# Kernel tuning notes

Hardware: AMD Instinct MI355X
Metric: run time of the kernel (lower is better)

Reference implementation:

```python
import jax, jax.numpy as jnp
import numpy as np

N_NODES = 50000
N_EDGES = 800000
IN_CH, HID, LAT = 256, 128, 64


def setup_inputs() -> dict:
    key = jax.random.key(0)
    k1, k2, k3, k4 = jax.random.split(key, 4)
    x = jax.random.normal(k1, (N_NODES, IN_CH), dtype=jnp.float32)
    edge_index = jax.random.randint(k2, (2, N_EDGES), 0, N_NODES, dtype=jnp.int64)
    W1 = jax.random.normal(k3, (IN_CH, HID), dtype=jnp.float32) * (1.0 / np.sqrt(IN_CH))
    b1 = jnp.zeros((HID,), dtype=jnp.float32)
    W2 = jax.random.normal(k4, (HID, LAT), dtype=jnp.float32) * (1.0 / np.sqrt(HID))
    b2 = jnp.zeros((LAT,), dtype=jnp.float32)
    return {"x": x, "edge_index": edge_index, "W1": W1, "b1": b1, "W2": W2, "b2": b2}


def gcn_conv(x, src, dst, deg_inv_sqrt, W, b):
    # PyG GCNConv: h = x @ W; out[dst] += d_dst^-1/2 * d_src^-1/2 * h[src]; + bias
    h = x @ W                                   # [N, out]
    norm = deg_inv_sqrt[src] * deg_inv_sqrt[dst]  # [E+N]
    msg = h[src] * norm[:, None]                # [E+N, out] (gather + scale)
    out = jax.ops.segment_sum(msg, dst, num_segments=x.shape[0])
    return out + b


def reference(x, edge_index, W1, b1, W2, b2):
    n = x.shape[0]
    loop = jnp.arange(n, dtype=edge_index.dtype)
    # add self loops (GCNConv default)
    src = jnp.concatenate([edge_index[0], loop])
    dst = jnp.concatenate([edge_index[1], loop])
    deg = jax.ops.segment_sum(jnp.ones_like(dst, dtype=x.dtype), dst, num_segments=n)
    deg_inv_sqrt = jnp.where(deg > 0, jax.lax.rsqrt(deg), 0.0)
    h = jax.nn.relu(gcn_conv(x, src, dst, deg_inv_sqrt, W1, b1))
    h = jax.nn.relu(gcn_conv(h, src, dst, deg_inv_sqrt, W2, b2))
    return h
```

## Files before the change

### kernel.cpp

```cpp
#include <hip/hip_runtime.h>

#define N_NODES 50000
#define N_EDGES 800000
#define IN_CH 256
#define HID 128
#define LAT 64
#define CAP 64
#define NBIN 196
#define BINCAP 4864

typedef __attribute__((ext_vector_type(8))) short short8;
typedef __attribute__((ext_vector_type(16))) float f32x16;

static __device__ __forceinline__ unsigned short bf16_rne(float x) {
    unsigned u = __float_as_uint(x);
    unsigned r = (u + 0x7FFFu + ((u >> 16) & 1u)) >> 16;
    return (unsigned short)r;
}
static __device__ __forceinline__ float bf16_to_f(unsigned short h) {
    return __uint_as_float(((unsigned)h) << 16);
}

static __device__ __forceinline__ void add8(uint4 p, float* a) {
    a[0] += __uint_as_float(p.x << 16);
    a[1] += __uint_as_float(p.x & 0xFFFF0000u);
    a[2] += __uint_as_float(p.y << 16);
    a[3] += __uint_as_float(p.y & 0xFFFF0000u);
    a[4] += __uint_as_float(p.z << 16);
    a[5] += __uint_as_float(p.z & 0xFFFF0000u);
    a[6] += __uint_as_float(p.w << 16);
    a[7] += __uint_as_float(p.w & 0xFFFF0000u);
}
static __device__ __forceinline__ void fma8(uint4 p, float m, float* a) {
    a[0] = fmaf(m, __uint_as_float(p.x << 16), a[0]);
    a[1] = fmaf(m, __uint_as_float(p.x & 0xFFFF0000u), a[1]);
    a[2] = fmaf(m, __uint_as_float(p.y << 16), a[2]);
    a[3] = fmaf(m, __uint_as_float(p.y & 0xFFFF0000u), a[3]);
    a[4] = fmaf(m, __uint_as_float(p.z << 16), a[4]);
    a[5] = fmaf(m, __uint_as_float(p.z & 0xFFFF0000u), a[5]);
    a[6] = fmaf(m, __uint_as_float(p.w << 16), a[6]);
    a[7] = fmaf(m, __uint_as_float(p.w & 0xFFFF0000u), a[7]);
}

template <int K, int NN>
static __device__ __forceinline__ void split_store(const float* __restrict__ W,
                                                   unsigned short* __restrict__ Wf, int i) {
    constexpr int CT = NN / 32;
    int k = i / NN, n = i % NN;
    float w = W[i];
    unsigned short hi = bf16_rne(w);
    unsigned short lo = bf16_rne(w - bf16_to_f(hi));
    size_t off = ((size_t)((k >> 4) * CT + (n >> 5)) * 64 + ((n & 31) + 32 * ((k >> 3) & 1))) * 8 + (k & 7);
    Wf[off] = hi;
    Wf[(size_t)K * NN + off] = lo;
}

__global__ __launch_bounds__(256) void prep_kernel(const float* __restrict__ W1,
                                                   const float* __restrict__ W2,
                                                   int* __restrict__ binCnt,
                                                   unsigned short* __restrict__ W1f,
                                                   unsigned short* __restrict__ W2f) {
    int i = blockIdx.x * blockDim.x + threadIdx.x;
    if (i < NBIN) binCnt[i] = 0;
    if (i < IN_CH * HID) split_store<IN_CH, HID>(W1, W1f, i);
    if (i < HID * LAT) split_store<HID, LAT>(W2, W2f, i);
}

__global__ __launch_bounds__(256) void fill1_kernel(const int* __restrict__ ei,
                                                    int* __restrict__ binCnt,
                                                    unsigned int* __restrict__ binBuf, int E) {
    __shared__ int hist[NBIN];
    __shared__ int base[NBIN];
    const int tid = threadIdx.x;
    for (int i = tid; i < NBIN; i += 256) hist[i] = 0;
    __syncthreads();

    const int e0 = blockIdx.x * 2048 + tid;
    unsigned int pk[8];
    int bn[8], ofs[8];
#pragma unroll
    for (int i = 0; i < 8; ++i) {
        int e = e0 + 256 * i;
        bool v = e < E;
        int s = v ? ei[e] : 0;
        int d = v ? ei[E + e] : 0;
        bn[i] = d >> 8;
        pk[i] = (unsigned int)s | ((unsigned int)(d & 255) << 16);
        ofs[i] = v ? atomicAdd(&hist[bn[i]], 1) : -1;
    }
    __syncthreads();
    for (int i = tid; i < NBIN; i += 256)
        base[i] = hist[i] ? atomicAdd(&binCnt[i], hist[i]) : 0;
    __syncthreads();
#pragma unroll
    for (int i = 0; i < 8; ++i) {
        if (ofs[i] >= 0) {
            int p = base[bn[i]] + ofs[i];
            if (p < BINCAP) binBuf[(size_t)bn[i] * BINCAP + p] = pk[i];
        }
    }
}

__global__ __launch_bounds__(256) void fill2_kernel(const int* __restrict__ binCnt,
                                                    const unsigned int* __restrict__ binBuf,
                                                    int* __restrict__ cnt,
                                                    unsigned short* __restrict__ colb) {
    __shared__ int lcnt[256];
    const int b = blockIdx.x;
    const int tid = threadIdx.x;
    lcnt[tid] = 0;
    __syncthreads();
    int n = binCnt[b]; if (n > BINCAP) n = BINCAP;
    const int node0 = b << 8;
    const unsigned int* bb = binBuf + (size_t)b * BINCAP;
    int n4 = n & ~3;
    for (int i = tid * 4; i < n4; i += 1024) {
        uint4 pk4 = *(const uint4*)(bb + i);
        unsigned int pks[4] = {pk4.x, pk4.y, pk4.z, pk4.w};
#pragma unroll
        for (int q = 0; q < 4; ++q) {
            unsigned int pk = pks[q];
            int local = pk >> 16;
            int s = pk & 0xFFFF;
            int slot = atomicAdd(&lcnt[local], 1);
            if (slot < CAP) colb[(size_t)(node0 + local) * CAP + slot] = (unsigned short)s;
        }
    }
    for (int i = n4 + tid; i < n; i += 256) {
        unsigned int pk = bb[i];
        int local = pk >> 16;
        int s = pk & 0xFFFF;
        int slot = atomicAdd(&lcnt[local], 1);
        if (slot < CAP) colb[(size_t)(node0 + local) * CAP + slot] = (unsigned short)s;
    }
    __syncthreads();
    int node = node0 + tid;
    if (node < N_NODES) cnt[node] = lcnt[tid];
}

template <int K, int NN, bool AFP32>
__global__ __launch_bounds__(256) void gemm_kernel(const void* __restrict__ Av,
                                                   const unsigned short* __restrict__ Wf,
                                                   const int* __restrict__ cnt,
                                                   unsigned short* __restrict__ C, int M) {
    constexpr int CT = NN / 32;
    constexpr int NT = (NN == 128) ? 2 : 1;
    __shared__ unsigned short As[4 * 512];
    __shared__ unsigned short Bs[2 * 2 * CT * 512];

    const int tid = threadIdx.x;
    const int lane = tid & 63;
    const int w = tid >> 6;
    const int row0 = blockIdx.x * 64;
    const int rt = w >> 1;
    const int ct0 = (NN == 128) ? ((w & 1) * 2) : (w & 1);

    f32x16 acc[NT];
#pragma unroll
    for (int nt = 0; nt < NT; ++nt)
#pragma unroll
        for (int q = 0; q < 16; ++q) acc[nt][q] = 0.0f;

    for (int kt = 0; kt < K; kt += 32) {
        {
            int m = tid >> 2, kc = tid & 3;
            int row = row0 + m; if (row >= M) row = M - 1;
            int s = kc >> 1, half = kc & 1, t = m >> 5;
            int ln = (m & 31) + 32 * half;
            uint4 v;
            if constexpr (AFP32) {
                const float* A = (const float*)Av;
                const float4 v0 = *(const float4*)(A + (size_t)row * K + kt + kc * 8);
                const float4 v1 = *(const float4*)(A + (size_t)row * K + kt + kc * 8 + 4);
                v.x = (unsigned)bf16_rne(v0.x) | ((unsigned)bf16_rne(v0.y) << 16);
                v.y = (unsigned)bf16_rne(v0.z) | ((unsigned)bf16_rne(v0.w) << 16);
                v.z = (unsigned)bf16_rne(v1.x) | ((unsigned)bf16_rne(v1.y) << 16);
                v.w = (unsigned)bf16_rne(v1.z) | ((unsigned)bf16_rne(v1.w) << 16);
            } else {
                const unsigned short* A = (const unsigned short*)Av;
                v = *(const uint4*)(A + (size_t)row * K + kt + kc * 8);
            }
            *(uint4*)&As[((s * 2 + t) << 9) + (ln << 3)] = v;
        }
        {
            const int sg0 = kt >> 4;
#pragma unroll
            for (int i0 = 0; i0 < CT * 256; i0 += 256) {
                int i = i0 + tid;
                int psl = i / (CT * 64), rem = i % (CT * 64);
                int p = psl >> 1, sl = psl & 1;
                const uint4* src = (const uint4*)(Wf + (size_t)p * K * NN + (size_t)(sg0 + sl) * CT * 512);
                ((uint4*)Bs)[i] = src[rem];
            }
        }
        __syncthreads();

#pragma unroll
        for (int sl = 0; sl < 2; ++sl) {
            short8 a = *(const short8*)&As[((sl * 2 + rt) << 9) + (lane << 3)];
            short8 bh[NT], bl[NT];
#pragma unroll
            for (int nt = 0; nt < NT; ++nt) {
                bh[nt] = *(const short8*)&Bs[((sl * CT + ct0 + nt) << 9) + (lane << 3)];
                bl[nt] = *(const short8*)&Bs[(((2 + sl) * CT + ct0 + nt) << 9) + (lane << 3)];
            }
#pragma unroll
            for (int nt = 0; nt < NT; ++nt) {
                acc[nt] = __builtin_amdgcn_mfma_f32_32x32x16_bf16(a, bh[nt], acc[nt], 0, 0, 0);
                acc[nt] = __builtin_amdgcn_mfma_f32_32x32x16_bf16(a, bl[nt], acc[nt], 0, 0, 0);
            }
        }
        __syncthreads();
    }

#pragma unroll
    for (int r = 0; r < 16; ++r) {
        int rowl = rt * 32 + (r & 3) + 8 * (r >> 2) + 4 * (lane >> 5);
        int row = row0 + rowl;
        if (row < M) {
            float sc = rsqrtf((float)cnt[row] + 1.0f);
#pragma unroll
            for (int nt = 0; nt < NT; ++nt) {
                int col = (ct0 + nt) * 32 + (lane & 31);
                C[(size_t)row * NN + col] = bf16_rne(acc[nt][r] * sc);
            }
        }
    }
}

template <int C, bool OBF16>
__global__ __launch_bounds__(256) void agg_kernel(const int* __restrict__ cnt,
                                                  const unsigned short* __restrict__ colb,
                                                  const unsigned short* __restrict__ hs,
                                                  const float* __restrict__ bias,
                                                  void* __restrict__ outv, int N) {
    constexpr int LPN = C / 8;
    constexpr int NPW = 64 / LPN;
    int node = (int)((blockIdx.x * blockDim.x + threadIdx.x) >> 6);
    int lane = threadIdx.x & 63;
    if (node >= N) return;
    const int g = lane / LPN;
    const int c = lane % LPN;

    int deg = cnt[node];
    int kk = deg < CAP ? deg : CAP;

    float acc[8];
#pragma unroll
    for (int q = 0; q < 8; ++q) acc[q] = 0.0f;
    if (g == 0) add8(*(const uint4*)(hs + (size_t)node * C + c * 8), acc);

    int myc = (lane < kk) ? (int)colb[(size_t)node * CAP + lane] : 0;

    int j = 0;
    for (; j + NPW * 4 <= kk; j += NPW * 4) {
        int s0 = __shfl(myc, j + g);
        int s1 = __shfl(myc, j + g + NPW);
        int s2 = __shfl(myc, j + g + 2 * NPW);
        int s3 = __shfl(myc, j + g + 3 * NPW);
        uint4 p0 = *(const uint4*)(hs + (size_t)s0 * C + c * 8);
        uint4 p1 = *(const uint4*)(hs + (size_t)s1 * C + c * 8);
        uint4 p2 = *(const uint4*)(hs + (size_t)s2 * C + c * 8);
        uint4 p3 = *(const uint4*)(hs + (size_t)s3 * C + c * 8);
        add8(p0, acc); add8(p1, acc); add8(p2, acc); add8(p3, acc);
    }
    if (j < kk) {
        bool v0 = (j + g) < kk, v1 = (j + g + NPW) < kk,
             v2 = (j + g + 2 * NPW) < kk, v3 = (j + g + 3 * NPW) < kk;
        int s0 = __shfl(myc, v0 ? (j + g) : 0);
        int s1 = __shfl(myc, v1 ? (j + g + NPW) : 0);
        int s2 = __shfl(myc, v2 ? (j + g + 2 * NPW) : 0);
        int s3 = __shfl(myc, v3 ? (j + g + 3 * NPW) : 0);
        uint4 p0 = *(const uint4*)(hs + (size_t)s0 * C + c * 8);
        uint4 p1 = *(const uint4*)(hs + (size_t)s1 * C + c * 8);
        uint4 p2 = *(const uint4*)(hs + (size_t)s2 * C + c * 8);
        uint4 p3 = *(const uint4*)(hs + (size_t)s3 * C + c * 8);
        fma8(p0, v0 ? 1.0f : 0.0f, acc);
        fma8(p1, v1 ? 1.0f : 0.0f, acc);
        fma8(p2, v2 ? 1.0f : 0.0f, acc);
        fma8(p3, v3 ? 1.0f : 0.0f, acc);
    }

#pragma unroll
    for (int s = LPN; s < 64; s <<= 1)
#pragma unroll
        for (int q = 0; q < 8; ++q) acc[q] += __shfl_xor(acc[q], s);

    if (lane < LPN) {
        float di = rsqrtf((float)deg + 1.0f);
        float o[8];
#pragma unroll
        for (int q = 0; q < 8; ++q)
            o[q] = fmaxf(fmaf(di, acc[q], bias[c * 8 + q]), 0.0f);
        if constexpr (OBF16) {
            unsigned short* out = (unsigned short*)outv;
            ushort4 lo4 = make_ushort4(bf16_rne(o[0]), bf16_rne(o[1]), bf16_rne(o[2]), bf16_rne(o[3]));
            ushort4 hi4 = make_ushort4(bf16_rne(o[4]), bf16_rne(o[5]), bf16_rne(o[6]), bf16_rne(o[7]));
            *(ushort4*)(out + (size_t)node * C + c * 8) = lo4;
            *(ushort4*)(out + (size_t)node * C + c * 8 + 4) = hi4;
        } else {
            float* out = (float*)outv;
            float4 o0 = {o[0], o[1], o[2], o[3]};
            float4 o1 = {o[4], o[5], o[6], o[7]};
            *(float4*)(out + (size_t)node * C + c * 8) = o0;
            *(float4*)(out + (size_t)node * C + c * 8 + 4) = o1;
        }
    }
}

extern "C" void kernel_launch(void* const* d_in, const int* in_sizes, int n_in,
                              void* d_out, int out_size, void* d_ws, size_t ws_size,
                              hipStream_t stream) {
    const float* x  = (const float*)d_in[0];
    const int*   ei = (const int*)d_in[1];
    const float* W1 = (const float*)d_in[2];
    const float* b1 = (const float*)d_in[3];
    const float* W2 = (const float*)d_in[4];
    const float* b2 = (const float*)d_in[5];

    const int N = N_NODES, E = N_EDGES;

    char* ws = (char*)d_ws;
    size_t off = 0;
    auto alloc = [&](size_t bytes) {
        void* p = ws + off;
        off = (off + bytes + 255) & ~(size_t)255;
        return p;
    };
    int*            cnt    = (int*)alloc((size_t)N * 4);
    unsigned short* colb   = (unsigned short*)alloc((size_t)N * CAP * 2);
    int*            binCnt = (int*)alloc((size_t)NBIN * 4);
    unsigned int*   binBuf = (unsigned int*)alloc((size_t)NBIN * BINCAP * 4);
    unsigned short* W1f    = (unsigned short*)alloc((size_t)2 * IN_CH * HID * 2);
    unsigned short* W2f    = (unsigned short*)alloc((size_t)2 * HID * LAT * 2);
    unsigned short* h1s    = (unsigned short*)alloc((size_t)N * HID * 2);
    unsigned short* act1   = (unsigned short*)alloc((size_t)N * HID * 2);
    unsigned short* h2s    = h1s;

    prep_kernel<<<(N + 255) / 256, 256, 0, stream>>>(W1, W2, binCnt, W1f, W2f);
    fill1_kernel<<<(E + 2047) / 2048, 256, 0, stream>>>(ei, binCnt, binBuf, E);
    fill2_kernel<<<NBIN, 256, 0, stream>>>(binCnt, binBuf, cnt, colb);

    gemm_kernel<IN_CH, HID, true><<<(N + 63) / 64, 256, 0, stream>>>(x, W1f, cnt, h1s, N);
    agg_kernel<HID, true><<<(N + 3) / 4, 256, 0, stream>>>(cnt, colb, h1s, b1, act1, N);

    gemm_kernel<HID, LAT, false><<<(N + 63) / 64, 256, 0, stream>>>(act1, W2f, cnt, h2s, N);
    agg_kernel<LAT, false><<<(N + 3) / 4, 256, 0, stream>>>(cnt, colb, h2s, b2, d_out, N);
}
```

Before: 195.9 us.

## Fold weight prep into fill1, split fill2 bins in halves, hoist agg loads

Removes the separate prep kernel: the bin counter is cleared with a memset and the weight hi/lo bf16 split is done inside fill1, which now handles 1024 edges per block for more blocks. fill2 launches two blocks per bin, each handling half the destination nodes, to double parallelism, though each block still reads the whole bin and discards half. The aggregation kernel issues the self-row and column-index loads before reading the degree so their latencies overlap. Fill1 now needs at least as many threads as the weight count (782 blocks cover 32768 elements, which holds).

Measured after the change: 198.2 us. About the same (+1.2%).

```diff
diff --git a/kernel.cpp b/kernel.cpp
--- a/kernel.cpp
+++ b/kernel.cpp
@@ -8,6 +8,7 @@
 #define CAP 64
 #define NBIN 196
 #define BINCAP 4864
+#define EPB 1024
 
 typedef __attribute__((ext_vector_type(8))) short short8;
 typedef __attribute__((ext_vector_type(16))) float f32x16;
@@ -55,31 +56,28 @@
     Wf[(size_t)K * NN + off] = lo;
 }
 
-__global__ __launch_bounds__(256) void prep_kernel(const float* __restrict__ W1,
-                                                   const float* __restrict__ W2,
-                                                   int* __restrict__ binCnt,
-                                                   unsigned short* __restrict__ W1f,
-                                                   unsigned short* __restrict__ W2f) {
-    int i = blockIdx.x * blockDim.x + threadIdx.x;
-    if (i < NBIN) binCnt[i] = 0;
-    if (i < IN_CH * HID) split_store<IN_CH, HID>(W1, W1f, i);
-    if (i < HID * LAT) split_store<HID, LAT>(W2, W2f, i);
-}
-
 __global__ __launch_bounds__(256) void fill1_kernel(const int* __restrict__ ei,
+                                                    const float* __restrict__ W1,
+                                                    const float* __restrict__ W2,
+                                                    unsigned short* __restrict__ W1f,
+                                                    unsigned short* __restrict__ W2f,
                                                     int* __restrict__ binCnt,
                                                     unsigned int* __restrict__ binBuf, int E) {
     __shared__ int hist[NBIN];
     __shared__ int base[NBIN];
     const int tid = threadIdx.x;
+    const int gtid = blockIdx.x * 256 + tid;
+    if (gtid < IN_CH * HID) split_store<IN_CH, HID>(W1, W1f, gtid);
+    if (gtid < HID * LAT) split_store<HID, LAT>(W2, W2f, gtid);
+
     for (int i = tid; i < NBIN; i += 256) hist[i] = 0;
     __syncthreads();
 
-    const int e0 = blockIdx.x * 2048 + tid;
-    unsigned int pk[8];
-    int bn[8], ofs[8];
-#pragma unroll
-    for (int i = 0; i < 8; ++i) {
+    const int e0 = blockIdx.x * EPB + tid;
+    unsigned int pk[EPB / 256];
+    int bn[EPB / 256], ofs[EPB / 256];
+#pragma unroll
+    for (int i = 0; i < EPB / 256; ++i) {
         int e = e0 + 256 * i;
         bool v = e < E;
         int s = v ? ei[e] : 0;
@@ -93,7 +91,7 @@
         base[i] = hist[i] ? atomicAdd(&binCnt[i], hist[i]) : 0;
     __syncthreads();
 #pragma unroll
-    for (int i = 0; i < 8; ++i) {
+    for (int i = 0; i < EPB / 256; ++i) {
         if (ofs[i] >= 0) {
             int p = base[bn[i]] + ofs[i];
             if (p < BINCAP) binBuf[(size_t)bn[i] * BINCAP + p] = pk[i];
@@ -105,10 +103,11 @@
                                                     const unsigned int* __restrict__ binBuf,
                                                     int* __restrict__ cnt,
                                                     unsigned short* __restrict__ colb) {
-    __shared__ int lcnt[256];
-    const int b = blockIdx.x;
+    __shared__ int lcnt[128];
+    const int b = blockIdx.x >> 1;
+    const int half = blockIdx.x & 1;
     const int tid = threadIdx.x;
-    lcnt[tid] = 0;
+    if (tid < 128) lcnt[tid] = 0;
     __syncthreads();
     int n = binCnt[b]; if (n > BINCAP) n = BINCAP;
     const int node0 = b << 8;
@@ -121,21 +120,25 @@
         for (int q = 0; q < 4; ++q) {
             unsigned int pk = pks[q];
             int local = pk >> 16;
+            if ((local >> 7) != half) continue;
             int s = pk & 0xFFFF;
-            int slot = atomicAdd(&lcnt[local], 1);
+            int slot = atomicAdd(&lcnt[local & 127], 1);
             if (slot < CAP) colb[(size_t)(node0 + local) * CAP + slot] = (unsigned short)s;
         }
     }
     for (int i = n4 + tid; i < n; i += 256) {
         unsigned int pk = bb[i];
         int local = pk >> 16;
+        if ((local >> 7) != half) continue;
         int s = pk & 0xFFFF;
-        int slot = atomicAdd(&lcnt[local], 1);
+        int slot = atomicAdd(&lcnt[local & 127], 1);
         if (slot < CAP) colb[(size_t)(node0 + local) * CAP + slot] = (unsigned short)s;
     }
     __syncthreads();
-    int node = node0 + tid;
-    if (node < N_NODES) cnt[node] = lcnt[tid];
+    if (tid < 128) {
+        int node = node0 + (half << 7) + tid;
+        if (node < N_NODES) cnt[node] = lcnt[tid];
+    }
 }
 
 template <int K, int NN, bool AFP32>
@@ -242,15 +245,17 @@
     const int g = lane / LPN;
     const int c = lane % LPN;
 
+    uint4 selfp = *(const uint4*)(hs + (size_t)node * C + c * 8);
+    int rawc = (int)colb[(size_t)node * CAP + lane];
     int deg = cnt[node];
     int kk = deg < CAP ? deg : CAP;
 
     float acc[8];
 #pragma unroll
     for (int q = 0; q < 8; ++q) acc[q] = 0.0f;
-    if (g == 0) add8(*(const uint4*)(hs + (size_t)node * C + c * 8), acc);
-
-    int myc = (lane < kk) ? (int)colb[(size_t)node * CAP + lane] : 0;
+    if (g == 0) add8(selfp, acc);
+
+    int myc = (lane < kk) ? rawc : 0;
 
     int j = 0;
     for (; j + NPW * 4 <= kk; j += NPW * 4) {
@@ -337,9 +342,9 @@
     unsigned short* act1   = (unsigned short*)alloc((size_t)N * HID * 2);
     unsigned short* h2s    = h1s;
 
-    prep_kernel<<<(N + 255) / 256, 256, 0, stream>>>(W1, W2, binCnt, W1f, W2f);
-    fill1_kernel<<<(E + 2047) / 2048, 256, 0, stream>>>(ei, binCnt, binBuf, E);
-    fill2_kernel<<<NBIN, 256, 0, stream>>>(binCnt, binBuf, cnt, colb);
+    hipMemsetAsync(binCnt, 0, (size_t)NBIN * 4, stream);
+    fill1_kernel<<<(E + EPB - 1) / EPB, 256, 0, stream>>>(ei, W1, W2, W1f, W2f, binCnt, binBuf, E);
+    fill2_kernel<<<NBIN * 2, 256, 0, stream>>>(binCnt, binBuf, cnt, colb);
 
     gemm_kernel<IN_CH, HID, true><<<(N + 63) / 64, 256, 0, stream>>>(x, W1f, cnt, h1s, N);
     agg_kernel<HID, true><<<(N + 3) / 4, 256, 0, stream>>>(cnt, colb, h1s, b1, act1, N);
```

## Store hidden features as 32-column planes and aggregate plane by plane

Applied to the files above, without the earlier changes.

The GEMM now writes its bf16 output in a planar layout, with 32-column slices stored contiguously per node. The second GEMM reads its A operand from that same layout. Aggregation is split into one pass per 32-column plane, launched as a grid over chunk times node blocks. Each pass gathers 64-byte rows from a plane that is a quarter or half the size, which improves cache locality for the random neighbour gathers. The cost is that the neighbour indices and degrees are re-read once per plane and there are more blocks to launch.

Result: slower. 255.5 us (+30.4%).

```diff
diff --git a/kernel.cpp b/kernel.cpp
--- a/kernel.cpp
+++ b/kernel.cpp
@@ -178,7 +178,7 @@
                 v.w = (unsigned)bf16_rne(v1.z) | ((unsigned)bf16_rne(v1.w) << 16);
             } else {
                 const unsigned short* A = (const unsigned short*)Av;
-                v = *(const uint4*)(A + (size_t)row * K + kt + kc * 8);
+                v = *(const uint4*)(A + ((size_t)(kt >> 5) * M + row) * 32 + kc * 8);
             }
             *(uint4*)&As[((s * 2 + t) << 9) + (ln << 3)] = v;
         }
@@ -221,89 +221,76 @@
             float sc = rsqrtf((float)cnt[row] + 1.0f);
 #pragma unroll
             for (int nt = 0; nt < NT; ++nt) {
-                int col = (ct0 + nt) * 32 + (lane & 31);
-                C[(size_t)row * NN + col] = bf16_rne(acc[nt][r] * sc);
+                int p = ct0 + nt;
+                C[((size_t)p * M + row) * 32 + (lane & 31)] = bf16_rne(acc[nt][r] * sc);
             }
         }
     }
 }
 
 template <int C, bool OBF16>
-__global__ __launch_bounds__(256) void agg_kernel(const int* __restrict__ cnt,
-                                                  const unsigned short* __restrict__ colb,
-                                                  const unsigned short* __restrict__ hs,
-                                                  const float* __restrict__ bias,
-                                                  void* __restrict__ outv, int N) {
-    constexpr int LPN = C / 8;
-    constexpr int NPW = 64 / LPN;
-    int node = (int)((blockIdx.x * blockDim.x + threadIdx.x) >> 6);
-    int lane = threadIdx.x & 63;
+__global__ __launch_bounds__(256) void aggc_kernel(const int* __restrict__ cnt,
+                                                   const unsigned short* __restrict__ colb,
+                                                   const unsigned short* __restrict__ hs,
+                                                   const float* __restrict__ bias,
+                                                   void* __restrict__ outv, int N) {
+    constexpr int NB = (N_NODES + 3) / 4;
+    const int chunk = blockIdx.x / NB;
+    const int node = (blockIdx.x % NB) * 4 + (threadIdx.x >> 6);
+    const int lane = threadIdx.x & 63;
     if (node >= N) return;
-    const int g = lane / LPN;
-    const int c = lane % LPN;
-
+    const int g = lane >> 2;
+    const int c = lane & 3;
+
+    const unsigned short* plane = hs + (size_t)chunk * N * 32;
+
+    uint4 selfp = *(const uint4*)(plane + (size_t)node * 32 + c * 8);
+    int rawc = (int)colb[(size_t)node * CAP + lane];
     int deg = cnt[node];
     int kk = deg < CAP ? deg : CAP;
 
     float acc[8];
 #pragma unroll
     for (int q = 0; q < 8; ++q) acc[q] = 0.0f;
-    if (g == 0) add8(*(const uint4*)(hs + (size_t)node * C + c * 8), acc);
-
-    int myc = (lane < kk) ? (int)colb[(size_t)node * CAP + lane] : 0;
-
-    int j = 0;
-    for (; j + NPW * 4 <= kk; j += NPW * 4) {
-        int s0 = __shfl(myc, j + g);
-        int s1 = __shfl(myc, j + g + NPW);
-        int s2 = __shfl(myc, j + g + 2 * NPW);
-        int s3 = __shfl(myc, j + g + 3 * NPW);
-        uint4 p0 = *(const uint4*)(hs + (size_t)s0 * C + c * 8);
-        uint4 p1 = *(const uint4*)(hs + (size_t)s1 * C + c * 8);
-        uint4 p2 = *(const uint4*)(hs + (size_t)s2 * C + c * 8);
-        uint4 p3 = *(const uint4*)(hs + (size_t)s3 * C + c * 8);
-        add8(p0, acc); add8(p1, acc); add8(p2, acc); add8(p3, acc);
-    }
-    if (j < kk) {
-        bool v0 = (j + g) < kk, v1 = (j + g + NPW) < kk,
-             v2 = (j + g + 2 * NPW) < kk, v3 = (j + g + 3 * NPW) < kk;
+    if (g == 0) add8(selfp, acc);
+
+    int myc = (lane < kk) ? rawc : 0;
+
+    for (int j = 0; j < kk; j += 32) {
+        bool v0 = (j + g) < kk, v1 = (j + g + 16) < kk;
         int s0 = __shfl(myc, v0 ? (j + g) : 0);
-        int s1 = __shfl(myc, v1 ? (j + g + NPW) : 0);
-        int s2 = __shfl(myc, v2 ? (j + g + 2 * NPW) : 0);
-        int s3 = __shfl(myc, v3 ? (j + g + 3 * NPW) : 0);
-        uint4 p0 = *(const uint4*)(hs + (size_t)s0 * C + c * 8);
-        uint4 p1 = *(const uint4*)(hs + (size_t)s1 * C + c * 8);
-        uint4 p2 = *(const uint4*)(hs + (size_t)s2 * C + c * 8);
-        uint4 p3 = *(const uint4*)(hs + (size_t)s3 * C + c * 8);
+        int s1 = __shfl(myc, v1 ? (j + g + 16) : 0);
+        uint4 p0 = *(const uint4*)(plane + (size_t)s0 * 32 + c * 8);
+        uint4 p1 = *(const uint4*)(plane + (size_t)s1 * 32 + c * 8);
         fma8(p0, v0 ? 1.0f : 0.0f, acc);
         fma8(p1, v1 ? 1.0f : 0.0f, acc);
-        fma8(p2, v2 ? 1.0f : 0.0f, acc);
-        fma8(p3, v3 ? 1.0f : 0.0f, acc);
-    }
-
-#pragma unroll
-    for (int s = LPN; s < 64; s <<= 1)
+    }
+
+#pragma unroll
+    for (int s = 4; s < 64; s <<= 1)
 #pragma unroll
         for (int q = 0; q < 8; ++q) acc[q] += __shfl_xor(acc[q], s);
 
-    if (lane < LPN) {
+    if (lane < 4) {
         float di = rsqrtf((float)deg + 1.0f);
         float o[8];
 #pragma unroll
         for (int q = 0; q < 8; ++q)
-            o[q] = fmaxf(fmaf(di, acc[q], bias[c * 8 + q]), 0.0f);
+            o[q] = fmaxf(fmaf(di, acc[q], bias[chunk * 32 + c * 8 + q]), 0.0f);
         if constexpr (OBF16) {
             unsigned short* out = (unsigned short*)outv;
+            unsigned short* op = out + ((size_t)chunk * N + node) * 32 + c * 8;
             ushort4 lo4 = make_ushort4(bf16_rne(o[0]), bf16_rne(o[1]), bf16_rne(o[2]), bf16_rne(o[3]));
             ushort4 hi4 = make_ushort4(bf16_rne(o[4]), bf16_rne(o[5]), bf16_rne(o[6]), bf16_rne(o[7]));
-            *(ushort4*)(out + (size_t)node * C + c * 8) = lo4;
-            *(ushort4*)(out + (size_t)node * C + c * 8 + 4) = hi4;
+            *(ushort4*)op = lo4;
+            *(ushort4*)(op + 4) = hi4;
         } else {
             float* out = (float*)outv;
+            float* op = out + (size_t)node * C + chunk * 32 + c * 8;
             float4 o0 = {o[0], o[1], o[2], o[3]};
             float4 o1 = {o[4], o[5], o[6], o[7]};
-            *(float4*)(out + (size_t)node * C + c * 8) = o0;
-            *(float4*)(out + (size_t)node * C + c * 8 + 4) = o1;
+            *(float4*)op = o0;
+            *(float4*)(op + 4) = o1;
         }
     }
 }
@@ -319,6 +306,7 @@
     const float* b2 = (const float*)d_in[5];
 
     const int N = N_NODES, E = N_EDGES;
+    const int NB = (N_NODES + 3) / 4;
 
     char* ws = (char*)d_ws;
     size_t off = 0;
@@ -342,8 +330,8 @@
     fill2_kernel<<<NBIN, 256, 0, stream>>>(binCnt, binBuf, cnt, colb);
 
     gemm_kernel<IN_CH, HID, true><<<(N + 63) / 64, 256, 0, stream>>>(x, W1f, cnt, h1s, N);
-    agg_kernel<HID, true><<<(N + 3) / 4, 256, 0, stream>>>(cnt, colb, h1s, b1, act1, N);
+    aggc_kernel<HID, true><<<4 * NB, 256, 0, stream>>>(cnt, colb, h1s, b1, act1, N);
 
     gemm_kernel<HID, LAT, false><<<(N + 63) / 64, 256, 0, stream>>>(act1, W2f, cnt, h2s, N);
-    agg_kernel<LAT, false><<<(N + 3) / 4, 256, 0, stream>>>(cnt, colb, h2s, b2, d_out, N);
-}
+    aggc_kernel<LAT, false><<<2 * NB, 256, 0, stream>>>(cnt, colb, h2s, b2, d_out, N);
+}
```

## Map aggregation to LPN lanes per node instead of a wavefront per node

Applied to the files above, without the earlier changes.

The aggregation kernel now gives each node a small group of lanes (C/8 lanes, one per 8-channel chunk) instead of a full 64-lane wavefront. Each thread walks the node's neighbour list directly with vector index loads, so the shuffle-based index broadcast and the cross-lane reduction are gone. Grid size grows in node count per block accordingly. This cuts reduction and shuffle overhead and idle lanes, but each thread now runs a longer serial gather loop, and nodes of differing degree share a wavefront, which can cause divergence.

Result: faster. 190.5 us, median of 2 (-2.8%).

```diff
diff --git a/kernel.cpp b/kernel.cpp
--- a/kernel.cpp
+++ b/kernel.cpp
@@ -235,76 +235,72 @@
                                                   const float* __restrict__ bias,
                                                   void* __restrict__ outv, int N) {
     constexpr int LPN = C / 8;
-    constexpr int NPW = 64 / LPN;
-    int node = (int)((blockIdx.x * blockDim.x + threadIdx.x) >> 6);
-    int lane = threadIdx.x & 63;
+    constexpr int NPB = 256 / LPN;
+    const int node = blockIdx.x * NPB + (int)(threadIdx.x / LPN);
+    const int u = threadIdx.x % LPN;
     if (node >= N) return;
-    const int g = lane / LPN;
-    const int c = lane % LPN;
-
+
+    const unsigned short* __restrict__ hbase = hs + u * 8;
+
+    uint4 selfp = *(const uint4*)(hbase + (size_t)node * C);
     int deg = cnt[node];
+    const unsigned short* __restrict__ cb = colb + (size_t)node * CAP;
     int kk = deg < CAP ? deg : CAP;
 
     float acc[8];
 #pragma unroll
     for (int q = 0; q < 8; ++q) acc[q] = 0.0f;
-    if (g == 0) add8(*(const uint4*)(hs + (size_t)node * C + c * 8), acc);
-
-    int myc = (lane < kk) ? (int)colb[(size_t)node * CAP + lane] : 0;
+    add8(selfp, acc);
 
     int j = 0;
-    for (; j + NPW * 4 <= kk; j += NPW * 4) {
-        int s0 = __shfl(myc, j + g);
-        int s1 = __shfl(myc, j + g + NPW);
-        int s2 = __shfl(myc, j + g + 2 * NPW);
-        int s3 = __shfl(myc, j + g + 3 * NPW);
-        uint4 p0 = *(const uint4*)(hs + (size_t)s0 * C + c * 8);
-        uint4 p1 = *(const uint4*)(hs + (size_t)s1 * C + c * 8);
-        uint4 p2 = *(const uint4*)(hs + (size_t)s2 * C + c * 8);
-        uint4 p3 = *(const uint4*)(hs + (size_t)s3 * C + c * 8);
+    for (; j + 4 <= kk; j += 4) {
+        ushort4 s4 = *(const ushort4*)(cb + j);
+        uint4 p0 = *(const uint4*)(hbase + (size_t)s4.x * C);
+        uint4 p1 = *(const uint4*)(hbase + (size_t)s4.y * C);
+        uint4 p2 = *(const uint4*)(hbase + (size_t)s4.z * C);
+        uint4 p3 = *(const uint4*)(hbase + (size_t)s4.w * C);
         add8(p0, acc); add8(p1, acc); add8(p2, acc); add8(p3, acc);
     }
     if (j < kk) {
-        bool v0 = (j + g) < kk, v1 = (j + g + NPW) < kk,
-             v2 = (j + g + 2 * NPW) < kk, v3 = (j + g + 3 * NPW) < kk;
-        int s0 = __shfl(myc, v0 ? (j + g) : 0);
-        int s1 = __shfl(myc, v1 ? (j + g + NPW) : 0);
-        int s2 = __shfl(myc, v2 ? (j + g + 2 * NPW) : 0);
-        int s3 = __shfl(myc, v3 ? (j + g + 3 * NPW) : 0);
-        uint4 p0 = *(const uint4*)(hs + (size_t)s0 * C + c * 8);
-        uint4 p1 = *(const uint4*)(hs + (size_t)s1 * C + c * 8);
-        uint4 p2 = *(const uint4*)(hs + (size_t)s2 * C + c * 8);
-        uint4 p3 = *(const uint4*)(hs + (size_t)s3 * C + c * 8);
-        fma8(p0, v0 ? 1.0f : 0.0f, acc);
+        ushort4 s4 = *(const ushort4*)(cb + j);
+        bool v1 = (j + 1) < kk, v2 = (j + 2) < kk;
+        int t0 = s4.x;
+        int t1 = v1 ? (int)s4.y : 0;
+        int t2 = v2 ? (int)s4.z : 0;
+        uint4 p0 = *(const uint4*)(hbase + (size_t)t0 * C);
+        uint4 p1 = *(const uint4*)(hbase + (size_t)t1 * C);
+        uint4 p2 = *(const uint4*)(hbase + (size_t)t2 * C);
+        add8(p0, acc);
         fma8(p1, v1 ? 1.0f : 0.0f, acc);
         fma8(p2, v2 ? 1.0f : 0.0f, acc);
-        fma8(p3, v3 ? 1.0f : 0.0f, acc);
-    }
-
-#pragma unroll
-    for (int s = LPN; s < 64; s <<= 1)
-#pragma unroll
-        for (int q = 0; q < 8; ++q) acc[q] += __shfl_xor(acc[q], s);
-
-    if (lane < LPN) {
-        float di = rsqrtf((float)deg + 1.0f);
-        float o[8];
-#pragma unroll
-        for (int q = 0; q < 8; ++q)
-            o[q] = fmaxf(fmaf(di, acc[q], bias[c * 8 + q]), 0.0f);
-        if constexpr (OBF16) {
-            unsigned short* out = (unsigned short*)outv;
-            ushort4 lo4 = make_ushort4(bf16_rne(o[0]), bf16_rne(o[1]), bf16_rne(o[2]), bf16_rne(o[3]));
-            ushort4 hi4 = make_ushort4(bf16_rne(o[4]), bf16_rne(o[5]), bf16_rne(o[6]), bf16_rne(o[7]));
-            *(ushort4*)(out + (size_t)node * C + c * 8) = lo4;
-            *(ushort4*)(out + (size_t)node * C + c * 8 + 4) = hi4;
-        } else {
-            float* out = (float*)outv;
-            float4 o0 = {o[0], o[1], o[2], o[3]};
-            float4 o1 = {o[4], o[5], o[6], o[7]};
-            *(float4*)(out + (size_t)node * C + c * 8) = o0;
-            *(float4*)(out + (size_t)node * C + c * 8 + 4) = o1;
-        }
+    }
+
+    float di = rsqrtf((float)deg + 1.0f);
+    const float4 b0 = *(const float4*)(bias + u * 8);
+    const float4 b1 = *(const float4*)(bias + u * 8 + 4);
+    float o[8];
+    o[0] = fmaxf(fmaf(di, acc[0], b0.x), 0.0f);
+    o[1] = fmaxf(fmaf(di, acc[1], b0.y), 0.0f);
+    o[2] = fmaxf(fmaf(di, acc[2], b0.z), 0.0f);
+    o[3] = fmaxf(fmaf(di, acc[3], b0.w), 0.0f);
+    o[4] = fmaxf(fmaf(di, acc[4], b1.x), 0.0f);
+    o[5] = fmaxf(fmaf(di, acc[5], b1.y), 0.0f);
+    o[6] = fmaxf(fmaf(di, acc[6], b1.z), 0.0f);
+    o[7] = fmaxf(fmaf(di, acc[7], b1.w), 0.0f);
+
+    if constexpr (OBF16) {
+        uint4 st;
+        st.x = (unsigned)bf16_rne(o[0]) | ((unsigned)bf16_rne(o[1]) << 16);
+        st.y = (unsigned)bf16_rne(o[2]) | ((unsigned)bf16_rne(o[3]) << 16);
+        st.z = (unsigned)bf16_rne(o[4]) | ((unsigned)bf16_rne(o[5]) << 16);
+        st.w = (unsigned)bf16_rne(o[6]) | ((unsigned)bf16_rne(o[7]) << 16);
+        *(uint4*)((unsigned short*)outv + (size_t)node * C + u * 8) = st;
+    } else {
+        float* op = (float*)outv + (size_t)node * C + u * 8;
+        float4 o0 = {o[0], o[1], o[2], o[3]};
+        float4 o1 = {o[4], o[5], o[6], o[7]};
+        *(float4*)op = o0;
+        *(float4*)(op + 4) = o1;
     }
 }
 
@@ -342,8 +338,8 @@
     fill2_kernel<<<NBIN, 256, 0, stream>>>(binCnt, binBuf, cnt, colb);
 
     gemm_kernel<IN_CH, HID, true><<<(N + 63) / 64, 256, 0, stream>>>(x, W1f, cnt, h1s, N);
-    agg_kernel<HID, true><<<(N + 3) / 4, 256, 0, stream>>>(cnt, colb, h1s, b1, act1, N);
+    agg_kernel<HID, true><<<(N + 15) / 16, 256, 0, stream>>>(cnt, colb, h1s, b1, act1, N);
 
     gemm_kernel<HID, LAT, false><<<(N + 63) / 64, 256, 0, stream>>>(act1, W2f, cnt, h2s, N);
-    agg_kernel<LAT, false><<<(N + 3) / 4, 256, 0, stream>>>(cnt, colb, h2s, b2, d_out, N);
-}
+    agg_kernel<LAT, false><<<(N + 31) / 32, 256, 0, stream>>>(cnt, colb, h2s, b2, d_out, N);
+}
```
